# Performance work log

Measured on AMD Instinct MI355X. Metric: run time of the kernel, lower is better.

Reference implementation:

```python
import jax, jax.numpy as jnp
import numpy as np

B, T, C, H = 4, 2048, 1024, 16
D = C // H  # head_dim = 64


def setup_inputs() -> dict:
    key = jax.random.key(0)
    k1, k2, k3 = jax.random.split(key, 3)
    x = jax.random.normal(k1, (B, T, C), dtype=jnp.float32)
    w_attn = jax.random.normal(k2, (C, 3 * C), dtype=jnp.float32) * (1.0 / np.sqrt(C))
    b_attn = jnp.zeros((3 * C,), dtype=jnp.float32)
    w_proj = jax.random.normal(k3, (C, C), dtype=jnp.float32) * (1.0 / np.sqrt(C))
    b_proj = jnp.zeros((C,), dtype=jnp.float32)
    return {"x": x, "w_attn": w_attn, "b_attn": b_attn, "w_proj": w_proj, "b_proj": b_proj}


def reference(x, w_attn, b_attn, w_proj, b_proj):
    Bx, Tx, Cx = x.shape
    qkv = x @ w_attn + b_attn                      # (B, T, 3C)
    q, k, v = jnp.split(qkv, 3, axis=2)
    # (B, T, C) -> (B, H, T, D)
    q = q.reshape(Bx, Tx, H, D).transpose(0, 2, 1, 3)
    k = k.reshape(Bx, Tx, H, D).transpose(0, 2, 1, 3)
    v = v.reshape(Bx, Tx, H, D).transpose(0, 2, 1, 3)
    scores = jnp.einsum('bhqd,bhkd->bhqk', q, k) / jnp.sqrt(jnp.float32(D))
    causal = jnp.tril(jnp.ones((Tx, Tx), dtype=bool))
    scores = jnp.where(causal[None, None], scores, jnp.float32(-jnp.inf))
    probs = jax.nn.softmax(scores, axis=-1)
    out = jnp.einsum('bhqk,bhkd->bhqd', probs, v)  # (B, H, T, D)
    out = out.transpose(0, 2, 1, 3).reshape(Bx, Tx, Cx)
    return out @ w_proj + b_proj
```

## Files before the change

kernel.cpp:

```cpp
#include <hip/hip_runtime.h>

#define AS1 __attribute__((address_space(1)))
#define AS3 __attribute__((address_space(3)))

using bf16x8  = __attribute__((ext_vector_type(8))) __bf16;
using floatx4 = __attribute__((ext_vector_type(4))) float;

#define SCQ 0.18033688f

__device__ inline ushort f2b(float f) {
    __bf16 h = (__bf16)f;
    return __builtin_bit_cast(ushort, h);
}

__device__ inline unsigned cvtpk_bf16(float lo, float hi) {
    unsigned r;
    asm("v_cvt_pk_bf16_f32 %0, %1, %2" : "=v"(r) : "v"(lo), "v"(hi));
    return r;
}
__device__ inline void plswap32(unsigned& a, unsigned& b) {
    asm("v_permlane32_swap_b32 %0, %1" : "+v"(a), "+v"(b));
}
__device__ inline void plswap16(unsigned& a, unsigned& b) {
    asm("v_permlane16_swap_b32 %0, %1" : "+v"(a), "+v"(b));
}

__device__ inline bf16x8 pack_swap(floatx4 ej0, floatx4 ej1) {
    unsigned x0 = cvtpk_bf16(ej0[0], ej0[1]);
    unsigned x1 = cvtpk_bf16(ej0[2], ej0[3]);
    unsigned y0 = cvtpk_bf16(ej1[0], ej1[1]);
    unsigned y1 = cvtpk_bf16(ej1[2], ej1[3]);
    plswap32(x0, y0); plswap16(x0, y0);
    plswap32(x1, y1); plswap16(x1, y1);
    union { unsigned u[4]; bf16x8 v; } ua;
    ua.u[0] = x0; ua.u[1] = x1; ua.u[2] = y0; ua.u[3] = y1;
    return ua.v;
}

__global__ void k_prep(const float* __restrict__ x, ushort* __restrict__ xb,
                       const float* __restrict__ wa, ushort* __restrict__ waT,
                       const float* __restrict__ wp, ushort* __restrict__ wpT)
{
    __shared__ float tile[32][33];
    int blk = blockIdx.x;
    if (blk < 8192) {
        int i = (blk * 256 + threadIdx.x) * 4;
        float4 v = *(const float4*)(x + i);
        ushort4 o;
        o.x = f2b(v.x); o.y = f2b(v.y); o.z = f2b(v.z); o.w = f2b(v.w);
        *(ushort4*)(xb + i) = o;
        return;
    }
    const float* in; ushort* out; int R, Ncol, bx, by; float scale; int scale_cols;
    if (blk < 11264) {
        int idx = blk - 8192;
        in = wa; out = waT; R = 1024; Ncol = 3072;
        bx = idx % 96; by = idx / 96; scale = SCQ; scale_cols = 1024;
    } else {
        int idx = blk - 11264;
        in = wp; out = wpT; R = 1024; Ncol = 1024;
        bx = idx % 32; by = idx / 32; scale = 1.0f; scale_cols = 0;
    }
    int tx = threadIdx.x & 31, ty = threadIdx.x >> 5;
    int c0 = bx * 32, r0 = by * 32;
    for (int i = 0; i < 32; i += 8)
        tile[ty + i][tx] = in[(size_t)(r0 + ty + i) * Ncol + c0 + tx];
    __syncthreads();
    for (int i = 0; i < 32; i += 8) {
        int n = c0 + ty + i;
        float v = tile[tx][ty + i];
        if (n < scale_cols) v *= scale;
        out[(size_t)n * R + r0 + tx] = f2b(v);
    }
}

__global__ __launch_bounds__(256, 2) void k_gemm_bt(
    const ushort* __restrict__ A, const ushort* __restrict__ Bt,
    const float* __restrict__ bias, float* __restrict__ outv,
    int M, int N, int K)
{
    __shared__ __align__(16) ushort As[128 * 64];
    __shared__ __align__(16) ushort Bs[128 * 64];
    int tid = threadIdx.x;
    int m0 = blockIdx.y * 128, n0 = blockIdx.x * 128;
    int lane = tid & 63;
    int wm = (tid >> 7) * 64;
    int wn = ((tid >> 6) & 1) * 64;
    int lr = lane & 15, quad = lane >> 4;

    floatx4 acc[4][4] = {};
    const ushort* ags[4]; const ushort* bgs[4]; int sdst[4];
    #pragma unroll
    for (int it = 0; it < 4; ++it) {
        int slot = tid + 256 * it;
        int row = slot >> 3, ch = slot & 7;
        ags[it] = A  + (size_t)(m0 + row) * K + ch * 8;
        bgs[it] = Bt + (size_t)(n0 + row) * K + ch * 8;
        sdst[it] = slot * 8;
    }

    for (int kt = 0; kt < K; kt += 64) {
        #pragma unroll
        for (int it = 0; it < 4; ++it) {
            __builtin_amdgcn_global_load_lds((const AS1 unsigned int*)(ags[it] + kt),
                                             (AS3 unsigned int*)&As[sdst[it]], 16, 0, 0);
            __builtin_amdgcn_global_load_lds((const AS1 unsigned int*)(bgs[it] + kt),
                                             (AS3 unsigned int*)&Bs[sdst[it]], 16, 0, 0);
        }
        asm volatile("s_waitcnt vmcnt(0)" ::: "memory");
        __syncthreads();
        bf16x8 af[4][2], bf[4][2];
        #pragma unroll
        for (int i = 0; i < 4; ++i) {
            af[i][0] = *(const bf16x8*)&As[(wm + 16 * i + lr) * 64 + quad * 8];
            af[i][1] = *(const bf16x8*)&As[(wm + 16 * i + lr) * 64 + 32 + quad * 8];
        }
        #pragma unroll
        for (int j = 0; j < 4; ++j) {
            bf[j][0] = *(const bf16x8*)&Bs[(wn + 16 * j + lr) * 64 + quad * 8];
            bf[j][1] = *(const bf16x8*)&Bs[(wn + 16 * j + lr) * 64 + 32 + quad * 8];
        }
        #pragma unroll
        for (int i = 0; i < 4; ++i)
            #pragma unroll
            for (int j = 0; j < 4; ++j) {
                acc[i][j] = __builtin_amdgcn_mfma_f32_16x16x32_bf16(af[i][0], bf[j][0], acc[i][j], 0, 0, 0);
                acc[i][j] = __builtin_amdgcn_mfma_f32_16x16x32_bf16(af[i][1], bf[j][1], acc[i][j], 0, 0, 0);
            }
        __syncthreads();
    }

    #pragma unroll
    for (int j = 0; j < 4; ++j) {
        int col = n0 + wn + 16 * j + lr;
        float bv = bias[col];
        #pragma unroll
        for (int i = 0; i < 4; ++i) {
            int row = m0 + wm + 16 * i + quad * 4;
            #pragma unroll
            for (int r = 0; r < 4; ++r)
                outv[(size_t)(row + r) * N + col] = acc[i][j][r] + bv;
        }
    }
}

__global__ __launch_bounds__(256, 2) void k_gemm_qkv(
    const ushort* __restrict__ A, const ushort* __restrict__ Bt,
    const float* __restrict__ bias, ushort* __restrict__ qkv, ushort* __restrict__ vt)
{
    constexpr int K = 1024;
    __shared__ __align__(16) ushort As[128 * 64];
    __shared__ __align__(16) ushort Bs[128 * 64];
    int tid = threadIdx.x;
    int m0 = blockIdx.y * 128, n0 = blockIdx.x * 128;
    int lane = tid & 63;
    int wm = (tid >> 7) * 64;
    int wn = ((tid >> 6) & 1) * 64;
    int lr = lane & 15, quad = lane >> 4;

    floatx4 acc[4][4] = {};
    const ushort* ags[4]; const ushort* bgs[4]; int sdst[4];
    #pragma unroll
    for (int it = 0; it < 4; ++it) {
        int slot = tid + 256 * it;
        int row = slot >> 3, ch = slot & 7;
        ags[it] = A  + (size_t)(m0 + row) * K + ch * 8;
        bgs[it] = Bt + (size_t)(n0 + row) * K + ch * 8;
        sdst[it] = slot * 8;
    }

    for (int kt = 0; kt < K; kt += 64) {
        #pragma unroll
        for (int it = 0; it < 4; ++it) {
            __builtin_amdgcn_global_load_lds((const AS1 unsigned int*)(ags[it] + kt),
                                             (AS3 unsigned int*)&As[sdst[it]], 16, 0, 0);
            __builtin_amdgcn_global_load_lds((const AS1 unsigned int*)(bgs[it] + kt),
                                             (AS3 unsigned int*)&Bs[sdst[it]], 16, 0, 0);
        }
        asm volatile("s_waitcnt vmcnt(0)" ::: "memory");
        __syncthreads();
        bf16x8 af[4][2], bf[4][2];
        #pragma unroll
        for (int i = 0; i < 4; ++i) {
            af[i][0] = *(const bf16x8*)&As[(wm + 16 * i + lr) * 64 + quad * 8];
            af[i][1] = *(const bf16x8*)&As[(wm + 16 * i + lr) * 64 + 32 + quad * 8];
        }
        #pragma unroll
        for (int j = 0; j < 4; ++j) {
            bf[j][0] = *(const bf16x8*)&Bs[(wn + 16 * j + lr) * 64 + quad * 8];
            bf[j][1] = *(const bf16x8*)&Bs[(wn + 16 * j + lr) * 64 + 32 + quad * 8];
        }
        #pragma unroll
        for (int i = 0; i < 4; ++i)
            #pragma unroll
            for (int j = 0; j < 4; ++j) {
                acc[i][j] = __builtin_amdgcn_mfma_f32_16x16x32_bf16(af[i][0], bf[j][0], acc[i][j], 0, 0, 0);
                acc[i][j] = __builtin_amdgcn_mfma_f32_16x16x32_bf16(af[i][1], bf[j][1], acc[i][j], 0, 0, 0);
            }
        __syncthreads();
    }

    int bb = m0 >> 11;
    #pragma unroll
    for (int j = 0; j < 4; ++j) {
        int col = n0 + wn + 16 * j + lr;
        float bv = bias[col];
        if (col < 1024) bv *= SCQ;
        if (col < 2048) {
            #pragma unroll
            for (int i = 0; i < 4; ++i) {
                int row = m0 + wm + 16 * i + quad * 4;
                #pragma unroll
                for (int r = 0; r < 4; ++r)
                    qkv[(size_t)(row + r) * 2048 + col] = f2b(acc[i][j][r] + bv);
            }
        } else {
            int h = (col - 2048) >> 6, d = (col - 2048) & 63;
            ushort* vbase = vt + ((size_t)(bb * 16 + h) * 64 + d) * 2048;
            #pragma unroll
            for (int i = 0; i < 4; ++i) {
                int t0 = (m0 + wm + 16 * i + quad * 4) & 2047;
                ushort4 pk;
                ((ushort*)&pk)[0] = f2b(acc[i][j][0] + bv);
                ((ushort*)&pk)[1] = f2b(acc[i][j][1] + bv);
                ((ushort*)&pk)[2] = f2b(acc[i][j][2] + bv);
                ((ushort*)&pk)[3] = f2b(acc[i][j][3] + bv);
                *(ushort4*)&vbase[t0] = pk;
            }
        }
    }
}

__global__ __launch_bounds__(512, 4) void k_attn(const ushort* __restrict__ qkv,
                                                 const ushort* __restrict__ vt,
                                                 ushort* __restrict__ out)
{
    constexpr int T = 2048, SQK = 2048, C = 1024;
    __shared__ __align__(16) ushort Ks[2][64 * 64];
    __shared__ __align__(16) ushort Vs[2][64 * 64];
    int tid = threadIdx.x;
    int lane = tid & 63, wave = tid >> 6;
    int lr = lane & 15, quad = lane >> 4, lk = quad * 8;
    int bh = blockIdx.y;
    int b = bh >> 4, h = bh & 15;
    size_t base = (size_t)b * T * SQK;
    const ushort* kg0 = qkv + base + 1024 + h * 64;
    const ushort* vg0 = vt + (size_t)bh * 64 * 2048;

    int srow = tid >> 3;
    int sg   = (tid & 7) ^ (srow & 7);
    int sdst = tid * 8;
    const ushort* kgs = kg0 + (size_t)srow * SQK + sg * 8;
    const ushort* vgs = vg0 + (size_t)srow * 2048 + sg * 8;

    bf16x8 ones;
    #pragma unroll
    for (int i = 0; i < 8; ++i) ones[i] = (__bf16)1.0f;
    int c0 = (quad ^ (lr & 7)) * 8;
    int c1 = ((4 + quad) ^ (lr & 7)) * 8;

    int qts[2] = { (int)blockIdx.x, 15 - (int)blockIdx.x };
    int cur = 0;
    for (int ti = 0; ti < 2; ++ti) {
        int qt = qts[ti];
        int qrow = qt * 128 + wave * 16;
        int kt_d = qrow >> 6;
        const ushort* qp = qkv + base + (size_t)(qrow + lr) * SQK + h * 64;
        bf16x8 aq0 = *(const bf16x8*)(qp + lk);
        bf16x8 aq1 = *(const bf16x8*)(qp + 32 + lk);
        floatx4 o[4] = {};
        floatx4 lacc = {};
        int ktmax = 2 * qt + 1;

        __builtin_amdgcn_global_load_lds((const AS1 unsigned int*)kgs,
                                         (AS3 unsigned int*)&Ks[cur][sdst], 16, 0, 0);
        __builtin_amdgcn_global_load_lds((const AS1 unsigned int*)vgs,
                                         (AS3 unsigned int*)&Vs[cur][sdst], 16, 0, 0);
        asm volatile("s_waitcnt vmcnt(0)" ::: "memory");
        __syncthreads();

        for (int kt = 0; kt <= ktmax; ++kt) {
            if (kt < ktmax) {
                __builtin_amdgcn_global_load_lds((const AS1 unsigned int*)(kgs + (size_t)(kt + 1) * 64 * SQK),
                                                 (AS3 unsigned int*)&Ks[cur ^ 1][sdst], 16, 0, 0);
                __builtin_amdgcn_global_load_lds((const AS1 unsigned int*)(vgs + (kt + 1) * 64),
                                                 (AS3 unsigned int*)&Vs[cur ^ 1][sdst], 16, 0, 0);
            }
            if (kt <= kt_d) {
                const ushort* Kb = Ks[cur];
                const ushort* Vb = Vs[cur];
                floatx4 s[4];
                #pragma unroll
                for (int j = 0; j < 4; ++j) {
                    const ushort* kr = &Kb[(16 * j + lr) * 64];
                    bf16x8 bk0 = *(const bf16x8*)(kr + c0);
                    bf16x8 bk1 = *(const bf16x8*)(kr + c1);
                    floatx4 z = {};
                    s[j] = __builtin_amdgcn_mfma_f32_16x16x32_bf16(bk0, aq0, z, 0, 0, 0);
                    s[j] = __builtin_amdgcn_mfma_f32_16x16x32_bf16(bk1, aq1, s[j], 0, 0, 0);
                }
                floatx4 e[4];
                if (kt == kt_d) {
                    int qa = qrow + lr;
                    #pragma unroll
                    for (int j = 0; j < 4; ++j)
                        #pragma unroll
                        for (int r = 0; r < 4; ++r)
                            e[j][r] = ((kt * 64 + 16 * j + quad * 4 + r) > qa) ? 0.f : exp2f(s[j][r]);
                } else {
                    #pragma unroll
                    for (int j = 0; j < 4; ++j)
                        #pragma unroll
                        for (int r = 0; r < 4; ++r)
                            e[j][r] = exp2f(s[j][r]);
                }
                bf16x8 ap0 = pack_swap(e[0], e[1]);
                bf16x8 ap1 = pack_swap(e[2], e[3]);
                lacc = __builtin_amdgcn_mfma_f32_16x16x32_bf16(ap0, ones, lacc, 0, 0, 0);
                lacc = __builtin_amdgcn_mfma_f32_16x16x32_bf16(ap1, ones, lacc, 0, 0, 0);
                #pragma unroll
                for (int jd = 0; jd < 4; ++jd) {
                    const ushort* vr = &Vb[(16 * jd + lr) * 64];
                    bf16x8 bv0 = *(const bf16x8*)(vr + c0);
                    bf16x8 bv1 = *(const bf16x8*)(vr + c1);
                    o[jd] = __builtin_amdgcn_mfma_f32_16x16x32_bf16(ap0, bv0, o[jd], 0, 0, 0);
                    o[jd] = __builtin_amdgcn_mfma_f32_16x16x32_bf16(ap1, bv1, o[jd], 0, 0, 0);
                }
            }
            asm volatile("s_waitcnt vmcnt(0)" ::: "memory");
            __syncthreads();
            cur ^= 1;
        }

        #pragma unroll
        for (int r = 0; r < 4; ++r) {
            float inv = 1.0f / lacc[r];
            int row = b * T + qrow + quad * 4 + r;
            #pragma unroll
            for (int jd = 0; jd < 4; ++jd)
                out[(size_t)row * C + h * 64 + 16 * jd + lr] = f2b(o[jd][r] * inv);
        }
    }
}

extern "C" void kernel_launch(void* const* d_in, const int* in_sizes, int n_in,
                              void* d_out, int out_size, void* d_ws, size_t ws_size,
                              hipStream_t stream) {
    const float* x      = (const float*)d_in[0];
    const float* w_attn = (const float*)d_in[1];
    const float* b_attn = (const float*)d_in[2];
    const float* w_proj = (const float*)d_in[3];
    const float* b_proj = (const float*)d_in[4];
    float* out = (float*)d_out;

    constexpr int Bb = 4, T = 2048, C = 1024;
    constexpr int M = Bb * T;

    ushort* xb  = (ushort*)d_ws;
    ushort* waT = xb  + (size_t)M * C;
    ushort* wpT = waT + (size_t)3 * C * C;
    ushort* qkv = wpT + (size_t)C * C;
    ushort* vt  = qkv + (size_t)M * 2 * C;
    ushort* ao  = vt  + (size_t)64 * 64 * T;

    k_prep<<<12288, 256, 0, stream>>>(x, xb, w_attn, waT, w_proj, wpT);
    k_gemm_qkv<<<dim3(3 * C / 128, M / 128), 256, 0, stream>>>(xb, waT, b_attn, qkv, vt);
    k_attn<<<dim3(8, Bb * 16), 512, 0, stream>>>(qkv, vt, ao);
    k_gemm_bt<<<dim3(C / 128, M / 128), 256, 0, stream>>>(ao, wpT, b_proj, out, M, C, C);
}
```

Before: 256.2 us.

## Deepen attention K/V prefetch to four LDS stages with raw exp and setprio

The attention kernel's K/V LDS ring grows from two stages to four, so tiles are prefetched three iterations ahead. Each iteration now waits only with a partial vmcnt count instead of draining all loads, hiding more global-load latency. exp2f is replaced by a raw v_exp_f32 instruction, which drops the compiler's range handling and relies on scores staying in range without denormal concerns. MFMA sections are wrapped in s_setprio to favour matrix issue across waves. The cost is twice the LDS per block, 64KB, which may reduce how many blocks fit per CU, plus an extra barrier per iteration.

New measurement: 244.1 us. -4.7%, faster.

```diff
diff --git a/kernel.cpp b/kernel.cpp
--- a/kernel.cpp
+++ b/kernel.cpp
@@ -11,6 +11,12 @@
 __device__ inline ushort f2b(float f) {
     __bf16 h = (__bf16)f;
     return __builtin_bit_cast(ushort, h);
+}
+
+__device__ inline float fexp2(float x) {
+    float r;
+    asm("v_exp_f32 %0, %1" : "=v"(r) : "v"(x));
+    return r;
 }
 
 __device__ inline unsigned cvtpk_bf16(float lo, float hi) {
@@ -236,8 +242,8 @@
                                                  ushort* __restrict__ out)
 {
     constexpr int T = 2048, SQK = 2048, C = 1024;
-    __shared__ __align__(16) ushort Ks[2][64 * 64];
-    __shared__ __align__(16) ushort Vs[2][64 * 64];
+    __shared__ __align__(16) ushort Ks[4][64 * 64];
+    __shared__ __align__(16) ushort Vs[4][64 * 64];
     int tid = threadIdx.x;
     int lane = tid & 63, wave = tid >> 6;
     int lr = lane & 15, quad = lane >> 4, lk = quad * 8;
@@ -260,7 +266,6 @@
     int c1 = ((4 + quad) ^ (lr & 7)) * 8;
 
     int qts[2] = { (int)blockIdx.x, 15 - (int)blockIdx.x };
-    int cur = 0;
     for (int ti = 0; ti < 2; ++ti) {
         int qt = qts[ti];
         int qrow = qt * 128 + wave * 16;
@@ -272,64 +277,90 @@
         floatx4 lacc = {};
         int ktmax = 2 * qt + 1;
 
+        __syncthreads();
+
         __builtin_amdgcn_global_load_lds((const AS1 unsigned int*)kgs,
-                                         (AS3 unsigned int*)&Ks[cur][sdst], 16, 0, 0);
+                                         (AS3 unsigned int*)&Ks[0][sdst], 16, 0, 0);
         __builtin_amdgcn_global_load_lds((const AS1 unsigned int*)vgs,
-                                         (AS3 unsigned int*)&Vs[cur][sdst], 16, 0, 0);
-        asm volatile("s_waitcnt vmcnt(0)" ::: "memory");
-        __syncthreads();
+                                         (AS3 unsigned int*)&Vs[0][sdst], 16, 0, 0);
+        if (ktmax >= 1) {
+            __builtin_amdgcn_global_load_lds((const AS1 unsigned int*)(kgs + (size_t)64 * SQK),
+                                             (AS3 unsigned int*)&Ks[1][sdst], 16, 0, 0);
+            __builtin_amdgcn_global_load_lds((const AS1 unsigned int*)(vgs + 64),
+                                             (AS3 unsigned int*)&Vs[1][sdst], 16, 0, 0);
+        }
+        if (ktmax >= 2) {
+            __builtin_amdgcn_global_load_lds((const AS1 unsigned int*)(kgs + (size_t)2 * 64 * SQK),
+                                             (AS3 unsigned int*)&Ks[2][sdst], 16, 0, 0);
+            __builtin_amdgcn_global_load_lds((const AS1 unsigned int*)(vgs + 2 * 64),
+                                             (AS3 unsigned int*)&Vs[2][sdst], 16, 0, 0);
+        }
 
         for (int kt = 0; kt <= ktmax; ++kt) {
-            if (kt < ktmax) {
-                __builtin_amdgcn_global_load_lds((const AS1 unsigned int*)(kgs + (size_t)(kt + 1) * 64 * SQK),
-                                                 (AS3 unsigned int*)&Ks[cur ^ 1][sdst], 16, 0, 0);
-                __builtin_amdgcn_global_load_lds((const AS1 unsigned int*)(vgs + (kt + 1) * 64),
-                                                 (AS3 unsigned int*)&Vs[cur ^ 1][sdst], 16, 0, 0);
-            }
-            if (kt <= kt_d) {
-                const ushort* Kb = Ks[cur];
-                const ushort* Vb = Vs[cur];
-                floatx4 s[4];
+            __syncthreads();
+            if (kt + 3 <= ktmax) {
+                int bidx = (kt + 3) & 3;
+                __builtin_amdgcn_global_load_lds((const AS1 unsigned int*)(kgs + (size_t)(kt + 3) * 64 * SQK),
+                                                 (AS3 unsigned int*)&Ks[bidx][sdst], 16, 0, 0);
+                __builtin_amdgcn_global_load_lds((const AS1 unsigned int*)(vgs + (kt + 3) * 64),
+                                                 (AS3 unsigned int*)&Vs[bidx][sdst], 16, 0, 0);
+                asm volatile("s_waitcnt vmcnt(6)" ::: "memory");
+            } else if (kt + 2 <= ktmax) {
+                asm volatile("s_waitcnt vmcnt(4)" ::: "memory");
+            } else if (kt + 1 <= ktmax) {
+                asm volatile("s_waitcnt vmcnt(2)" ::: "memory");
+            } else {
+                asm volatile("s_waitcnt vmcnt(0)" ::: "memory");
+            }
+            __syncthreads();
+
+            if (kt > kt_d) continue;
+            const ushort* Kb = Ks[kt & 3];
+            const ushort* Vb = Vs[kt & 3];
+
+            floatx4 s[4];
+            __builtin_amdgcn_s_setprio(1);
+            #pragma unroll
+            for (int j = 0; j < 4; ++j) {
+                const ushort* kr = &Kb[(16 * j + lr) * 64];
+                bf16x8 bk0 = *(const bf16x8*)(kr + c0);
+                bf16x8 bk1 = *(const bf16x8*)(kr + c1);
+                floatx4 z = {};
+                s[j] = __builtin_amdgcn_mfma_f32_16x16x32_bf16(bk0, aq0, z, 0, 0, 0);
+                s[j] = __builtin_amdgcn_mfma_f32_16x16x32_bf16(bk1, aq1, s[j], 0, 0, 0);
+            }
+            __builtin_amdgcn_s_setprio(0);
+
+            floatx4 e[4];
+            if (kt == kt_d) {
+                int qa = qrow + lr;
                 #pragma unroll
-                for (int j = 0; j < 4; ++j) {
-                    const ushort* kr = &Kb[(16 * j + lr) * 64];
-                    bf16x8 bk0 = *(const bf16x8*)(kr + c0);
-                    bf16x8 bk1 = *(const bf16x8*)(kr + c1);
-                    floatx4 z = {};
-                    s[j] = __builtin_amdgcn_mfma_f32_16x16x32_bf16(bk0, aq0, z, 0, 0, 0);
-                    s[j] = __builtin_amdgcn_mfma_f32_16x16x32_bf16(bk1, aq1, s[j], 0, 0, 0);
-                }
-                floatx4 e[4];
-                if (kt == kt_d) {
-                    int qa = qrow + lr;
+                for (int j = 0; j < 4; ++j)
                     #pragma unroll
-                    for (int j = 0; j < 4; ++j)
-                        #pragma unroll
-                        for (int r = 0; r < 4; ++r)
-                            e[j][r] = ((kt * 64 + 16 * j + quad * 4 + r) > qa) ? 0.f : exp2f(s[j][r]);
-                } else {
+                    for (int r = 0; r < 4; ++r)
+                        e[j][r] = ((kt * 64 + 16 * j + quad * 4 + r) > qa) ? 0.f : fexp2(s[j][r]);
+            } else {
+                #pragma unroll
+                for (int j = 0; j < 4; ++j)
                     #pragma unroll
-                    for (int j = 0; j < 4; ++j)
-                        #pragma unroll
-                        for (int r = 0; r < 4; ++r)
-                            e[j][r] = exp2f(s[j][r]);
-                }
-                bf16x8 ap0 = pack_swap(e[0], e[1]);
-                bf16x8 ap1 = pack_swap(e[2], e[3]);
-                lacc = __builtin_amdgcn_mfma_f32_16x16x32_bf16(ap0, ones, lacc, 0, 0, 0);
-                lacc = __builtin_amdgcn_mfma_f32_16x16x32_bf16(ap1, ones, lacc, 0, 0, 0);
-                #pragma unroll
-                for (int jd = 0; jd < 4; ++jd) {
-                    const ushort* vr = &Vb[(16 * jd + lr) * 64];
-                    bf16x8 bv0 = *(const bf16x8*)(vr + c0);
-                    bf16x8 bv1 = *(const bf16x8*)(vr + c1);
-                    o[jd] = __builtin_amdgcn_mfma_f32_16x16x32_bf16(ap0, bv0, o[jd], 0, 0, 0);
-                    o[jd] = __builtin_amdgcn_mfma_f32_16x16x32_bf16(ap1, bv1, o[jd], 0, 0, 0);
-                }
-            }
-            asm volatile("s_waitcnt vmcnt(0)" ::: "memory");
-            __syncthreads();
-            cur ^= 1;
+                    for (int r = 0; r < 4; ++r)
+                        e[j][r] = fexp2(s[j][r]);
+            }
+            bf16x8 ap0 = pack_swap(e[0], e[1]);
+            bf16x8 ap1 = pack_swap(e[2], e[3]);
+
+            __builtin_amdgcn_s_setprio(1);
+            lacc = __builtin_amdgcn_mfma_f32_16x16x32_bf16(ap0, ones, lacc, 0, 0, 0);
+            lacc = __builtin_amdgcn_mfma_f32_16x16x32_bf16(ap1, ones, lacc, 0, 0, 0);
+            #pragma unroll
+            for (int jd = 0; jd < 4; ++jd) {
+                const ushort* vr = &Vb[(16 * jd + lr) * 64];
+                bf16x8 bv0 = *(const bf16x8*)(vr + c0);
+                bf16x8 bv1 = *(const bf16x8*)(vr + c1);
+                o[jd] = __builtin_amdgcn_mfma_f32_16x16x32_bf16(ap0, bv0, o[jd], 0, 0, 0);
+                o[jd] = __builtin_amdgcn_mfma_f32_16x16x32_bf16(ap1, bv1, o[jd], 0, 0, 0);
+            }
+            __builtin_amdgcn_s_setprio(0);
         }
 
         #pragma unroll
```
